# Performance work log

Measured on AMD Instinct MI355X. Metric: run time of the kernel, lower is better.

Reference implementation:

```python
import jax, jax.numpy as jnp
import numpy as np

MIN_PS = 4
MAX_PS = 16


def _enforce(mb):
    # mb: (L,) bool candidate boundaries (merge_signal < 0.7-quantile)
    # Faithful re-implementation of _enforce_patch_size_constraints:
    # walk boundaries left->right, skip segments < MIN_PS (start not advanced),
    # accept otherwise, and insert ceil(ps/MAX_PS)-1 evenly spaced splits for
    # oversized segments. seq_len-1 is always appended as a candidate.
    L = mb.shape[0]
    pos = jnp.arange(L, dtype=jnp.int32)
    cand = mb | (pos == L - 1)

    def fwd_step(start, inp):
        p, is_c = inp
        ps = p - start
        acc = is_c & (ps >= MIN_PS)
        k = jnp.where(acc, (ps + MAX_PS - 1) // MAX_PS, jnp.int32(1))
        sz = jnp.maximum(jnp.where(acc, ps // k, jnp.int32(1)), 1)
        new_start = jnp.where(acc, p, start)
        return new_start, (acc, start, sz, k)

    _, (acc, seg_start, sz, k) = jax.lax.scan(fwd_step, jnp.int32(0), (pos, cand))

    # Reverse scan: propagate each accepted boundary's (start, split_size, num_splits)
    # back to the interior positions of its segment so splits can be placed in parallel.
    def rev_step(carry, inp):
        a, s, z, kk = inp
        cs, cz, ck, cv = carry
        out = (cs, cz, ck, cv)
        ncarry = (jnp.where(a, s, cs), jnp.where(a, z, cz), jnp.where(a, kk, ck), cv | a)
        return ncarry, out

    init = (jnp.int32(0), jnp.int32(1), jnp.int32(1), jnp.bool_(False))
    _, (fs, fz, fk, fv) = jax.lax.scan(rev_step, init, (acc, seg_start, sz, k), reverse=True)
    r = pos - fs
    j = r // fz
    split = fv & (r > 0) & (r % fz == 0) & (j >= 1) & (j <= fk - 1)
    return acc | split


def reference(x, attention_mask, W1, b1, W2, b2, Wc, bc, Wb1, bb1, Wb2, bb2):
    B, L, D = x.shape
    # content scorer: Linear -> ReLU -> Linear -> Sigmoid
    content = jax.nn.sigmoid(jax.nn.relu(x @ W1 + b1) @ W2 + b2)[..., 0]  # (B, L)
    # grouped Conv1d(d, d//2, k=3, pad=1, groups=d//4)
    xc = jnp.transpose(x, (0, 2, 1))  # (B, D, L)
    pf = jax.lax.conv_general_dilated(xc, Wc, (1,), ((1, 1),),
                                      feature_group_count=D // 4,
                                      dimension_numbers=('NCH', 'OIH', 'NCH'))
    pf = jnp.transpose(pf + bc[None, :, None], (0, 2, 1))  # (B, L, D//2)
    comb = jnp.concatenate([x, pf], axis=-1)
    bscore = jax.nn.sigmoid(jax.nn.relu(comb @ Wb1 + bb1) @ Wb2 + bb2)[..., 0]  # (B, L)
    signal = content * (1.0 - bscore) * attention_mask
    thr = jnp.quantile(signal, 0.7, axis=1, keepdims=True)
    mb = signal < thr
    new_b = jax.vmap(_enforce)(mb)  # (B, L) bool, new_b[:,0] is always False

    # segment id per token = inclusive cumsum of boundaries
    seg = jnp.cumsum(new_b.astype(jnp.int32), axis=1)
    seg_flat = (seg + jnp.arange(B, dtype=jnp.int32)[:, None] * L).reshape(-1)
    NS = B * L
    xm = x * attention_mask[..., None]
    e = jnp.sum(xm * xm, axis=-1).reshape(-1)  # softmax logits = ||token||^2
    m = jax.ops.segment_max(e, seg_flat, num_segments=NS)
    w = jnp.exp(e - m[seg_flat])
    denom = jax.ops.segment_sum(w, seg_flat, num_segments=NS)
    wn = w / denom[seg_flat]
    merged = jax.ops.segment_sum(xm.reshape(-1, D) * wn[:, None], seg_flat,
                                 num_segments=NS).reshape(B, L, D)
    # segment_boundaries: 1 for every segment except the first, zero padding
    n_last = seg[:, -1]
    p = jnp.arange(L)
    seg_bounds = ((p[None, :] >= 1) & (p[None, :] <= n_last[:, None])).astype(jnp.float32)
    return merged, seg_bounds


def setup_inputs() -> dict:
    key = jax.random.key(0)
    B, L, D = 4, 8192, 512
    ks = jax.random.split(key, 8)
    s = 0.02
    return {
        'x': jax.random.normal(ks[0], (B, L, D), jnp.float32),
        'attention_mask': jnp.ones((B, L), jnp.float32),
        'W1': jax.random.normal(ks[1], (D, D // 4), jnp.float32) * s,
        'b1': jnp.zeros((D // 4,), jnp.float32),
        'W2': jax.random.normal(ks[2], (D // 4, 1), jnp.float32) * s,
        'b2': jnp.zeros((1,), jnp.float32),
        'Wc': jax.random.normal(ks[3], (D // 2, 4, 3), jnp.float32) * s,
        'bc': jnp.zeros((D // 2,), jnp.float32),
        'Wb1': jax.random.normal(ks[4], (D + D // 2, D // 4), jnp.float32) * s,
        'bb1': jnp.zeros((D // 4,), jnp.float32),
        'Wb2': jax.random.normal(ks[5], (D // 4, 1), jnp.float32) * s,
        'bb2': jnp.zeros((1,), jnp.float32),
    }
```

## Files before the change

kernel.cpp:

```cpp
#include <hip/hip_runtime.h>
#include <math.h>

#define B_  4
#define L_  8192
#define D_  512
#define BL_ (B_*L_)
#define TOK 64
#define XS  68
#define KC  16
#define NCH (D_/KC)

__global__ __launch_bounds__(256, 2) void k_signal(
    const float* __restrict__ x, const float* __restrict__ mask,
    const float* __restrict__ W1, const float* __restrict__ b1,
    const float* __restrict__ W2, const float* __restrict__ b2,
    const float* __restrict__ Wc, const float* __restrict__ bc,
    const float* __restrict__ Wb1, const float* __restrict__ bb1,
    const float* __restrict__ Wb2, const float* __restrict__ bb2,
    float* __restrict__ signal, float* __restrict__ e)
{
  __shared__ float ws1[KC][128];
  __shared__ float wsb[KC][128];
  __shared__ float wsp[8][128];
  __shared__ float xt[KC][XS];
  __shared__ float pf[8][XS];

  const int t   = threadIdx.x;
  const int blk = blockIdx.x;
  const int b   = blk >> 7;
  const int l0  = (blk & 127) << 6;
  const float* xb = x + (size_t)b * L_ * D_;

  const int jq = t & 31, tw = t >> 5;
  const int j0 = jq << 2, tok0 = tw << 3;

  const int stok = t >> 2, skk = t & 3;
  const int oo_c = t >> 5;
  const int m2   = (t & 31) << 1;
  const int cb_c = (oo_c >> 1) << 2;

  const int srow = t >> 5, sc4 = (t & 31) << 2;

  float a1[8][4], a2[8][4];
#pragma unroll
  for (int i = 0; i < 8; ++i)
#pragma unroll
    for (int j = 0; j < 4; ++j) { a1[i][j] = 0.f; a2[i][j] = 0.f; }
  float esacc = 0.f;

  float4 r_w1a, r_w1b, r_wba, r_wbb, r_wp, r_xv, r_hv;
  float4 r_wc0, r_wc1, r_wc2;
  float  r_bc;

  auto LOAD = [&](int c) {
    const int kc = c << 4;
    r_w1a = *reinterpret_cast<const float4*>(W1  + (size_t)(kc + srow) * 128 + sc4);
    r_w1b = *reinterpret_cast<const float4*>(W1  + (size_t)(kc + 8 + srow) * 128 + sc4);
    r_wba = *reinterpret_cast<const float4*>(Wb1 + (size_t)(kc + srow) * 128 + sc4);
    r_wbb = *reinterpret_cast<const float4*>(Wb1 + (size_t)(kc + 8 + srow) * 128 + sc4);
    r_wp  = *reinterpret_cast<const float4*>(Wb1 + (size_t)(512 + (c << 3) + srow) * 128 + sc4);
    r_xv  = *reinterpret_cast<const float4*>(xb + (size_t)(l0 + stok) * D_ + kc + (skk << 2));
    if (t < 8) {
      const int hh = t >> 2, kk = t & 3;
      const int l = hh ? (l0 + TOK) : (l0 - 1);
      r_hv = make_float4(0.f, 0.f, 0.f, 0.f);
      if (l >= 0 && l < L_)
        r_hv = *reinterpret_cast<const float4*>(xb + (size_t)l * D_ + kc + (kk << 2));
    }
    const int o = (c << 3) + oo_c;
    const float* wcp = Wc + o * 12;
    r_wc0 = *reinterpret_cast<const float4*>(wcp);
    r_wc1 = *reinterpret_cast<const float4*>(wcp + 4);
    r_wc2 = *reinterpret_cast<const float4*>(wcp + 8);
    r_bc  = bc[o];
  };

  LOAD(0);

  for (int c = 0; c < NCH; ++c) {
    __syncthreads();

    *reinterpret_cast<float4*>(&ws1[srow][sc4])     = r_w1a;
    *reinterpret_cast<float4*>(&ws1[8 + srow][sc4]) = r_w1b;
    *reinterpret_cast<float4*>(&wsb[srow][sc4])     = r_wba;
    *reinterpret_cast<float4*>(&wsb[8 + srow][sc4]) = r_wbb;
    *reinterpret_cast<float4*>(&wsp[srow][sc4])     = r_wp;
    {
      const float4 v = r_xv;
      esacc = fmaf(v.x, v.x, esacc); esacc = fmaf(v.y, v.y, esacc);
      esacc = fmaf(v.z, v.z, esacc); esacc = fmaf(v.w, v.w, esacc);
      const int r = skk << 2;
      xt[r + 0][stok] = v.x; xt[r + 1][stok] = v.y;
      xt[r + 2][stok] = v.z; xt[r + 3][stok] = v.w;
    }
    if (t < 8) {
      const int hh = t >> 2, kk = t & 3;
      const int col = TOK + hh, r = kk << 2;
      xt[r + 0][col] = r_hv.x; xt[r + 1][col] = r_hv.y;
      xt[r + 2][col] = r_hv.z; xt[r + 3][col] = r_hv.w;
    }
    __syncthreads();

    float wcl[12];
    wcl[0] = r_wc0.x; wcl[1]  = r_wc0.y; wcl[2]  = r_wc0.z; wcl[3]  = r_wc0.w;
    wcl[4] = r_wc1.x; wcl[5]  = r_wc1.y; wcl[6]  = r_wc1.z; wcl[7]  = r_wc1.w;
    wcl[8] = r_wc2.x; wcl[9]  = r_wc2.y; wcl[10] = r_wc2.z; wcl[11] = r_wc2.w;
    const float bcv = r_bc;

    if (c + 1 < NCH) LOAD(c + 1);

    {
      float pa = bcv, pb = bcv;
      const int tm1 = (m2 == 0) ? TOK : m2 - 1;
      const int tp2 = (m2 + 2 == TOK) ? TOK + 1 : m2 + 2;
#pragma unroll
      for (int i = 0; i < 4; ++i) {
        const float* row = &xt[cb_c + i][0];
        const float  xm1 = row[tm1];
        const float2 x01 = *reinterpret_cast<const float2*>(&row[m2]);
        const float  xp2 = row[tp2];
        pa = fmaf(xm1,   wcl[i * 3 + 0], pa);
        pa = fmaf(x01.x, wcl[i * 3 + 1], pa);
        pa = fmaf(x01.y, wcl[i * 3 + 2], pa);
        pb = fmaf(x01.x, wcl[i * 3 + 0], pb);
        pb = fmaf(x01.y, wcl[i * 3 + 1], pb);
        pb = fmaf(xp2,   wcl[i * 3 + 2], pb);
      }
      *reinterpret_cast<float2*>(&pf[oo_c][m2]) = make_float2(pa, pb);
    }

#pragma unroll 4
    for (int k = 0; k < KC; ++k) {
      const float4 w1 = *reinterpret_cast<const float4*>(&ws1[k][j0]);
      const float4 wb = *reinterpret_cast<const float4*>(&wsb[k][j0]);
      const float4 xa = *reinterpret_cast<const float4*>(&xt[k][tok0]);
      const float4 xc = *reinterpret_cast<const float4*>(&xt[k][tok0 + 4]);
      const float xs8[8] = {xa.x, xa.y, xa.z, xa.w, xc.x, xc.y, xc.z, xc.w};
#pragma unroll
      for (int i = 0; i < 8; ++i) {
        a1[i][0] = fmaf(xs8[i], w1.x, a1[i][0]);
        a1[i][1] = fmaf(xs8[i], w1.y, a1[i][1]);
        a1[i][2] = fmaf(xs8[i], w1.z, a1[i][2]);
        a1[i][3] = fmaf(xs8[i], w1.w, a1[i][3]);
        a2[i][0] = fmaf(xs8[i], wb.x, a2[i][0]);
        a2[i][1] = fmaf(xs8[i], wb.y, a2[i][1]);
        a2[i][2] = fmaf(xs8[i], wb.z, a2[i][2]);
        a2[i][3] = fmaf(xs8[i], wb.w, a2[i][3]);
      }
    }
    __syncthreads();

#pragma unroll 2
    for (int oo = 0; oo < 8; ++oo) {
      const float4 wp = *reinterpret_cast<const float4*>(&wsp[oo][j0]);
      const float4 pa4 = *reinterpret_cast<const float4*>(&pf[oo][tok0]);
      const float4 pb4 = *reinterpret_cast<const float4*>(&pf[oo][tok0 + 4]);
      const float ps8[8] = {pa4.x, pa4.y, pa4.z, pa4.w, pb4.x, pb4.y, pb4.z, pb4.w};
#pragma unroll
      for (int i = 0; i < 8; ++i) {
        a2[i][0] = fmaf(ps8[i], wp.x, a2[i][0]);
        a2[i][1] = fmaf(ps8[i], wp.y, a2[i][1]);
        a2[i][2] = fmaf(ps8[i], wp.z, a2[i][2]);
        a2[i][3] = fmaf(ps8[i], wp.w, a2[i][3]);
      }
    }
  }

  {
    float b1v[4], w2v[4], bbv[4], wv2[4];
#pragma unroll
    for (int jj = 0; jj < 4; ++jj) {
      b1v[jj] = b1[j0 + jj];  w2v[jj] = W2[j0 + jj];
      bbv[jj] = bb1[j0 + jj]; wv2[jj] = Wb2[j0 + jj];
    }
    const float bias2 = b2[0], biasb2 = bb2[0];
#pragma unroll
    for (int i = 0; i < 8; ++i) {
      float p1 = 0.f, p2 = 0.f;
#pragma unroll
      for (int jj = 0; jj < 4; ++jj) {
        const float h1 = a1[i][jj] + b1v[jj];
        if (h1 > 0.f) p1 = fmaf(h1, w2v[jj], p1);
        const float h2 = a2[i][jj] + bbv[jj];
        if (h2 > 0.f) p2 = fmaf(h2, wv2[jj], p2);
      }
#pragma unroll
      for (int off = 1; off < 32; off <<= 1) {
        p1 += __shfl_xor(p1, off, 64);
        p2 += __shfl_xor(p2, off, 64);
      }
      if (jq == 0) {
        const int gi = b * L_ + l0 + tok0 + i;
        const float content = 1.f / (1.f + expf(-(p1 + bias2)));
        const float bscore  = 1.f / (1.f + expf(-(p2 + biasb2)));
        signal[gi] = content * (1.f - bscore) * mask[gi];
      }
    }
  }

  {
    float es = esacc;
    es += __shfl_xor(es, 1, 64);
    es += __shfl_xor(es, 2, 64);
    if (skk == 0) {
      const int gi = b * L_ + l0 + stok;
      const float m = mask[gi];
      e[gi] = m * m * es;
    }
  }
}

__device__ __forceinline__ int chain_sim(unsigned long long w, int from) {
  int last = -1;
  while (from < 64) {
    const unsigned long long m = w & (~0ull << from);
    if (m == 0ull) break;
    const int p = __ffsll(m) - 1;
    last = p;
    from = p + 4;
  }
  return last;
}

__global__ __launch_bounds__(1024) void k_select(
    const float* __restrict__ signal,
    int* __restrict__ starts, int* __restrict__ nlast)
{
  __shared__ unsigned int bins[4][256];
  __shared__ unsigned int sel_prefix;
  __shared__ int sel_rank;
  __shared__ float sh_thr;
  __shared__ unsigned int wmin[16];
  __shared__ int wcnt[16];
  __shared__ unsigned long long cw[128];
  __shared__ unsigned char nb[L_];
  __shared__ signed char tbl[128][4];
  __shared__ int st_in[128];
  __shared__ int offs[257];

  const int b = blockIdx.x, t = threadIdx.x;
  const int wv = t >> 6, lane = t & 63;
  const float* s = signal + b * L_;

  float val[8];
  unsigned int key[8];
#pragma unroll
  for (int i = 0; i < 8; ++i) {
    val[i] = s[(i << 10) + t];
    const unsigned int u = __float_as_uint(val[i]);
    key[i] = (u & 0x80000000u) ? ~u : (u | 0x80000000u);
  }

  if (t == 0) { sel_prefix = 0u; sel_rank = 5733; }
  __syncthreads();
  for (int round = 0; round < 4; ++round) {
    reinterpret_cast<unsigned int*>(bins)[t] = 0u;
    __syncthreads();
    const unsigned int pre = sel_prefix;
    const int shift = 24 - 8 * round;
#pragma unroll
    for (int i = 0; i < 8; ++i) {
      if (round == 0 || (key[i] >> (shift + 8)) == pre)
        atomicAdd(&bins[t >> 8][(key[i] >> shift) & 255u], 1u);
    }
    __syncthreads();
    if (t < 256)
      bins[0][t] = bins[0][t] + bins[1][t] + bins[2][t] + bins[3][t];
    __syncthreads();
    if (t < 64) {
      const unsigned int c0 = bins[0][(t << 2) + 0], c1 = bins[0][(t << 2) + 1];
      const unsigned int c2 = bins[0][(t << 2) + 2], c3 = bins[0][(t << 2) + 3];
      const unsigned int lsum = c0 + c1 + c2 + c3;
      unsigned int run = lsum;
#pragma unroll
      for (int off = 1; off < 64; off <<= 1) {
        const unsigned int v = __shfl_up(run, off, 64);
        if (t >= off) run += v;
      }
      const int r = sel_rank;
      if (r >= (int)(run - lsum) && r < (int)run) {
        int rr = r - (int)(run - lsum);
        unsigned int cbin;
        if (rr < (int)c0) { cbin = 0; }
        else if (rr < (int)(c0 + c1)) { cbin = 1; rr -= (int)c0; }
        else if (rr < (int)(c0 + c1 + c2)) { cbin = 2; rr -= (int)(c0 + c1); }
        else { cbin = 3; rr -= (int)(c0 + c1 + c2); }
        sel_rank = rr;
        sel_prefix = (pre << 8) | ((unsigned int)(t << 2) | cbin);
      }
    }
    __syncthreads();
  }
  const unsigned int k0 = sel_prefix;

  {
    int cle = 0;
    unsigned int mgt = 0xFFFFFFFFu;
#pragma unroll
    for (int i = 0; i < 8; ++i) {
      if (key[i] <= k0) ++cle;
      else mgt = min(mgt, key[i]);
    }
#pragma unroll
    for (int off = 1; off < 64; off <<= 1) {
      cle += __shfl_xor(cle, off, 64);
      mgt = min(mgt, (unsigned int)__shfl_xor((int)mgt, off, 64));
    }
    if (lane == 0) { wcnt[wv] = cle; wmin[wv] = mgt; }
    __syncthreads();
    if (t == 0) {
      int C = 0; unsigned int M = 0xFFFFFFFFu;
      for (int g = 0; g < 16; ++g) { C += wcnt[g]; M = min(M, wmin[g]); }
      const unsigned int k1 = (C >= 5735) ? k0 : M;
      const unsigned int u0 = (k0 & 0x80000000u) ? (k0 & 0x7fffffffu) : ~k0;
      const unsigned int u1 = (k1 & 0x80000000u) ? (k1 & 0x7fffffffu) : ~k1;
      const float v0 = __uint_as_float(u0);
      const float v1 = __uint_as_float(u1);
      const float g = 0.7f * 8191.0f - 5733.0f;
      sh_thr = v0 + g * (v1 - v0);
    }
    __syncthreads();
  }
  const float thr = sh_thr;

#pragma unroll
  for (int i = 0; i < 8; ++i) {
    const unsigned long long m = __ballot(val[i] < thr);
    if (lane == 0) cw[(i << 4) + wv] = m;
  }
  {
    const int base = t << 3;
#pragma unroll
    for (int i = 0; i < 8; ++i) nb[base + i] = 0;
  }
  __syncthreads();
  if (t == 0) cw[127] |= (1ull << 63);
  __syncthreads();

  if (t < 512) {
    const int blk = t >> 2, cls = t & 3;
    tbl[blk][cls] = (signed char)chain_sim(cw[blk], cls);
  }
  __syncthreads();

  if (t == 0) {
    int st = 0;
    for (int blk = 0; blk < 128; ++blk) {
      const int bs = blk << 6;
      st_in[blk] = st;
      int pl;
      if (blk == 0) {
        pl = chain_sim(cw[0], 4);
      } else {
        int off = st + 4 - bs;
        if (off < 0) off = 0;
        pl = tbl[blk][off];
      }
      if (pl >= 0) st = bs + pl;
    }
  }
  __syncthreads();

  if (t < 128) {
    const int bs = t << 6;
    const unsigned long long w = cw[t];
    int st = st_in[t];
    int from = st + 4 - bs;
    if (from < 0) from = 0;
    while (from < 64) {
      const unsigned long long m = w & (~0ull << from);
      if (m == 0ull) break;
      const int p_rel = __ffsll(m) - 1;
      const int p = bs + p_rel;
      nb[p] = 1;
      const int ps = p - st;
      const int k = (ps + 15) >> 4;
      if (k > 1) {
        int sz = ps / k; if (sz < 1) sz = 1;
        for (int j = 1; j < k; ++j) nb[st + j * sz] = 1;
      }
      st = p;
      from = p_rel + 4;
    }
  }
  __syncthreads();

  int ls = 0, run = 0;
  if (t < 256) {
    const int base = t << 5;
    for (int i = 0; i < 32; ++i) ls += nb[base + i];
    run = ls;
#pragma unroll
    for (int off = 1; off < 64; off <<= 1) {
      const int v = __shfl_up(run, off, 64);
      if ((t & 63) >= off) run += v;
    }
    if ((t & 63) == 63) wcnt[t >> 6] = run;
  }
  __syncthreads();
  if (t < 256) {
    const int w = t >> 6;
    int addb = 0;
    if (w > 0) addb += wcnt[0];
    if (w > 1) addb += wcnt[1];
    if (w > 2) addb += wcnt[2];
    offs[t] = addb + run - ls;
    if (t == 255) offs[256] = addb + run;
  }
  __syncthreads();
  if (t < 256) {
    const int base = t << 5;
    int rn = offs[t];
    for (int i = 0; i < 32; ++i) {
      rn += nb[base + i];
      if (nb[base + i]) starts[b * L_ + rn] = base + i;
    }
  }
  if (t == 0) { starts[b * L_ + 0] = 0; nlast[b] = offs[256]; }
}

__global__ __launch_bounds__(256) void k_merge(const float* __restrict__ x,
    const float* __restrict__ mask, const float* __restrict__ e,
    const int* __restrict__ starts, const int* __restrict__ nlast,
    float* __restrict__ merged, float* __restrict__ bounds)
{
  const int idx = (blockIdx.x << 2) + (threadIdx.x >> 6);
  const int b   = idx >> 13;
  const int sid = idx & (L_ - 1);
  const int n = nlast[b];
  const int lane = threadIdx.x & 63;
  if (lane == 0)
    bounds[(size_t)b * L_ + sid] = (sid >= 1 && sid <= n) ? 1.0f : 0.0f;
  const int c0 = lane << 3;
  float* o = merged + (size_t)(b * L_ + sid) * D_ + c0;
  if (sid > n) {
    const float4 z = make_float4(0.f, 0.f, 0.f, 0.f);
    reinterpret_cast<float4*>(o)[0] = z;
    reinterpret_cast<float4*>(o)[1] = z;
    return;
  }
  const int t0 = starts[b * L_ + sid];
  const int t1 = (sid < n) ? starts[b * L_ + sid + 1] : L_;
  const int len = t1 - t0;
  const float* eb = e + b * L_;

  float acc[8] = {0,0,0,0,0,0,0,0};

  if (len <= 64) {
    const float ev = (lane < len) ? eb[t0 + lane] : -INFINITY;
    float mx = ev;
#pragma unroll
    for (int off = 1; off < 64; off <<= 1)
      mx = fmaxf(mx, __shfl_xor(mx, off, 64));
    const float ex = expf(ev - mx);
    float den = ex;
#pragma unroll
    for (int off = 1; off < 64; off <<= 1)
      den += __shfl_xor(den, off, 64);
    const float mk = (lane < len) ? mask[b * L_ + t0 + lane] : 0.f;
    const float scl = (ex / den) * mk;

    const float* xr = x + (size_t)(b * L_ + t0) * D_ + c0;
    float4 u0 = reinterpret_cast<const float4*>(xr)[0];
    float4 u1 = reinterpret_cast<const float4*>(xr)[1];
    for (int r = 0; r < len; ++r) {
      float4 n0, n1;
      if (r + 1 < len) {
        const float* xn = xr + (size_t)(r + 1) * D_;
        n0 = reinterpret_cast<const float4*>(xn)[0];
        n1 = reinterpret_cast<const float4*>(xn)[1];
      }
      const float sc = __shfl(scl, r, 64);
      acc[0] = fmaf(sc, u0.x, acc[0]); acc[1] = fmaf(sc, u0.y, acc[1]);
      acc[2] = fmaf(sc, u0.z, acc[2]); acc[3] = fmaf(sc, u0.w, acc[3]);
      acc[4] = fmaf(sc, u1.x, acc[4]); acc[5] = fmaf(sc, u1.y, acc[5]);
      acc[6] = fmaf(sc, u1.z, acc[6]); acc[7] = fmaf(sc, u1.w, acc[7]);
      u0 = n0; u1 = n1;
    }
  } else {
    float mx = -INFINITY;
    for (int p = t0; p < t1; ++p) mx = fmaxf(mx, eb[p]);
    float den = 0.f;
    for (int p = t0; p < t1; ++p) den += expf(eb[p] - mx);
    for (int p = t0; p < t1; ++p) {
      const float wn = expf(eb[p] - mx) / den;
      const float sc = wn * mask[b * L_ + p];
      const float* xr = x + ((size_t)(b * L_ + p)) * D_ + c0;
      const float4 u0 = reinterpret_cast<const float4*>(xr)[0];
      const float4 u1 = reinterpret_cast<const float4*>(xr)[1];
      acc[0] = fmaf(sc, u0.x, acc[0]); acc[1] = fmaf(sc, u0.y, acc[1]);
      acc[2] = fmaf(sc, u0.z, acc[2]); acc[3] = fmaf(sc, u0.w, acc[3]);
      acc[4] = fmaf(sc, u1.x, acc[4]); acc[5] = fmaf(sc, u1.y, acc[5]);
      acc[6] = fmaf(sc, u1.z, acc[6]); acc[7] = fmaf(sc, u1.w, acc[7]);
    }
  }
  reinterpret_cast<float4*>(o)[0] = make_float4(acc[0], acc[1], acc[2], acc[3]);
  reinterpret_cast<float4*>(o)[1] = make_float4(acc[4], acc[5], acc[6], acc[7]);
}

extern "C" void kernel_launch(void* const* d_in, const int* in_sizes, int n_in,
                              void* d_out, int out_size, void* d_ws, size_t ws_size,
                              hipStream_t stream) {
  (void)in_sizes; (void)n_in; (void)out_size; (void)ws_size;
  const float* x    = (const float*)d_in[0];
  const float* mask = (const float*)d_in[1];
  const float* W1   = (const float*)d_in[2];
  const float* b1   = (const float*)d_in[3];
  const float* W2   = (const float*)d_in[4];
  const float* b2   = (const float*)d_in[5];
  const float* Wc   = (const float*)d_in[6];
  const float* bc   = (const float*)d_in[7];
  const float* Wb1  = (const float*)d_in[8];
  const float* bb1  = (const float*)d_in[9];
  const float* Wb2  = (const float*)d_in[10];
  const float* bb2  = (const float*)d_in[11];

  float* merged = (float*)d_out;
  float* bounds = (float*)d_out + (size_t)BL_ * D_;

  char* ws = (char*)d_ws;
  float* signal = (float*)(ws);
  float* e      = (float*)(ws + (size_t)BL_ * 4);
  int*   starts = (int*)  (ws + (size_t)BL_ * 8);
  int*   nlast  = (int*)  (ws + (size_t)BL_ * 12);

  k_signal<<<BL_ / TOK, 256, 0, stream>>>(x, mask, W1, b1, W2, b2, Wc, bc,
                                          Wb1, bb1, Wb2, bb2, signal, e);
  k_select<<<B_, 1024, 0, stream>>>(signal, starts, nlast);
  k_merge<<<BL_ / 4, 256, 0, stream>>>(x, mask, e, starts, nlast, merged, bounds);
}
```

Baseline: 301.5 us.

## Build top-byte histogram in signal kernel and pre-zero merged output there

The signal kernel now builds a per-batch histogram of the top radix byte of the signal keys in shared memory and adds it into a global histogram. This lets the select kernel skip its first radix-select round. The signal kernel also zero-fills its slice of the merged and bounds outputs while it computes, so the merge kernel can return early for padded segments instead of writing zeros. This moves the 64 MB zero-fill into a compute-bound kernel, where it may overlap with compute. The cost is a memset launch, extra global atomics, and extra store traffic during the signal kernel.

Measured after the change: 299.8 us. Within noise of the previous version (-0.6%).

```diff
diff --git a/kernel.cpp b/kernel.cpp
--- a/kernel.cpp
+++ b/kernel.cpp
@@ -17,7 +17,9 @@
     const float* __restrict__ Wc, const float* __restrict__ bc,
     const float* __restrict__ Wb1, const float* __restrict__ bb1,
     const float* __restrict__ Wb2, const float* __restrict__ bb2,
-    float* __restrict__ signal, float* __restrict__ e)
+    float* __restrict__ signal, float* __restrict__ e,
+    unsigned int* __restrict__ hist,
+    float* __restrict__ merged, float* __restrict__ bounds)
 {
   __shared__ float ws1[KC][128];
   __shared__ float wsb[KC][128];
@@ -40,6 +42,12 @@
   const int cb_c = (oo_c >> 1) << 2;
 
   const int srow = t >> 5, sc4 = (t & 31) << 2;
+
+  if (t < 16) {
+    float4* bz = reinterpret_cast<float4*>(bounds + (size_t)b * L_ + l0);
+    bz[t] = make_float4(0.f, 0.f, 0.f, 0.f);
+  }
+  float4* mz = reinterpret_cast<float4*>(merged + (size_t)(b * L_ + l0) * D_);
 
   float a1[8][4], a2[8][4];
 #pragma unroll
@@ -109,6 +117,8 @@
 
     if (c + 1 < NCH) LOAD(c + 1);
 
+    mz[(c << 8) + t] = make_float4(0.f, 0.f, 0.f, 0.f);
+
     {
       float pa = bcv, pb = bcv;
       const int tm1 = (m2 == 0) ? TOK : m2 - 1;
@@ -166,6 +176,9 @@
     }
   }
 
+  float sigv[8];
+#pragma unroll
+  for (int i = 0; i < 8; ++i) sigv[i] = 0.f;
   {
     float b1v[4], w2v[4], bbv[4], wv2[4];
 #pragma unroll
@@ -193,7 +206,9 @@
         const int gi = b * L_ + l0 + tok0 + i;
         const float content = 1.f / (1.f + expf(-(p1 + bias2)));
         const float bscore  = 1.f / (1.f + expf(-(p2 + biasb2)));
-        signal[gi] = content * (1.f - bscore) * mask[gi];
+        const float s = content * (1.f - bscore) * mask[gi];
+        sigv[i] = s;
+        signal[gi] = s;
       }
     }
   }
@@ -208,6 +223,24 @@
       e[gi] = m * m * es;
     }
   }
+
+  {
+    __syncthreads();
+    unsigned int* hl = reinterpret_cast<unsigned int*>(&xt[0][0]);
+    hl[t & 255] = 0u;
+    __syncthreads();
+    if (jq == 0) {
+#pragma unroll
+      for (int i = 0; i < 8; ++i) {
+        const unsigned int u = __float_as_uint(sigv[i]);
+        const unsigned int key = (u & 0x80000000u) ? ~u : (u | 0x80000000u);
+        atomicAdd(&hl[key >> 24], 1u);
+      }
+    }
+    __syncthreads();
+    const unsigned int cnt = hl[t & 255];
+    if (cnt) atomicAdd(&hist[(b << 8) + (t & 255)], cnt);
+  }
 }
 
 __device__ __forceinline__ int chain_sim(unsigned long long w, int from) {
@@ -223,7 +256,7 @@
 }
 
 __global__ __launch_bounds__(1024) void k_select(
-    const float* __restrict__ signal,
+    const float* __restrict__ signal, const unsigned int* __restrict__ hist,
     int* __restrict__ starts, int* __restrict__ nlast)
 {
   __shared__ unsigned int bins[4][256];
@@ -251,16 +284,40 @@
     key[i] = (u & 0x80000000u) ? ~u : (u | 0x80000000u);
   }
 
-  if (t == 0) { sel_prefix = 0u; sel_rank = 5733; }
-  __syncthreads();
-  for (int round = 0; round < 4; ++round) {
+  if (t < 256) bins[0][t] = hist[(b << 8) + t];
+  __syncthreads();
+  if (t < 64) {
+    const unsigned int c0 = bins[0][(t << 2) + 0], c1 = bins[0][(t << 2) + 1];
+    const unsigned int c2 = bins[0][(t << 2) + 2], c3 = bins[0][(t << 2) + 3];
+    const unsigned int lsum = c0 + c1 + c2 + c3;
+    unsigned int run = lsum;
+#pragma unroll
+    for (int off = 1; off < 64; off <<= 1) {
+      const unsigned int v = __shfl_up(run, off, 64);
+      if (t >= off) run += v;
+    }
+    const int r = 5733;
+    if (r >= (int)(run - lsum) && r < (int)run) {
+      int rr = r - (int)(run - lsum);
+      unsigned int cbin;
+      if (rr < (int)c0) { cbin = 0; }
+      else if (rr < (int)(c0 + c1)) { cbin = 1; rr -= (int)c0; }
+      else if (rr < (int)(c0 + c1 + c2)) { cbin = 2; rr -= (int)(c0 + c1); }
+      else { cbin = 3; rr -= (int)(c0 + c1 + c2); }
+      sel_rank = rr;
+      sel_prefix = (unsigned int)(t << 2) | cbin;
+    }
+  }
+  __syncthreads();
+
+  for (int round = 1; round < 4; ++round) {
     reinterpret_cast<unsigned int*>(bins)[t] = 0u;
     __syncthreads();
     const unsigned int pre = sel_prefix;
     const int shift = 24 - 8 * round;
 #pragma unroll
     for (int i = 0; i < 8; ++i) {
-      if (round == 0 || (key[i] >> (shift + 8)) == pre)
+      if ((key[i] >> (shift + 8)) == pre)
         atomicAdd(&bins[t >> 8][(key[i] >> shift) & 255u], 1u);
     }
     __syncthreads();
@@ -428,17 +485,12 @@
   const int b   = idx >> 13;
   const int sid = idx & (L_ - 1);
   const int n = nlast[b];
+  if (sid > n) return;
   const int lane = threadIdx.x & 63;
-  if (lane == 0)
-    bounds[(size_t)b * L_ + sid] = (sid >= 1 && sid <= n) ? 1.0f : 0.0f;
+  if (lane == 0 && sid >= 1)
+    bounds[(size_t)b * L_ + sid] = 1.0f;
   const int c0 = lane << 3;
   float* o = merged + (size_t)(b * L_ + sid) * D_ + c0;
-  if (sid > n) {
-    const float4 z = make_float4(0.f, 0.f, 0.f, 0.f);
-    reinterpret_cast<float4*>(o)[0] = z;
-    reinterpret_cast<float4*>(o)[1] = z;
-    return;
-  }
   const int t0 = starts[b * L_ + sid];
   const int t1 = (sid < n) ? starts[b * L_ + sid + 1] : L_;
   const int len = t1 - t0;
@@ -519,13 +571,16 @@
   float* bounds = (float*)d_out + (size_t)BL_ * D_;
 
   char* ws = (char*)d_ws;
-  float* signal = (float*)(ws);
-  float* e      = (float*)(ws + (size_t)BL_ * 4);
-  int*   starts = (int*)  (ws + (size_t)BL_ * 8);
-  int*   nlast  = (int*)  (ws + (size_t)BL_ * 12);
-
+  float*        signal = (float*)(ws);
+  float*        e      = (float*)(ws + (size_t)BL_ * 4);
+  int*          starts = (int*)  (ws + (size_t)BL_ * 8);
+  int*          nlast  = (int*)  (ws + (size_t)BL_ * 12);
+  unsigned int* hist   = (unsigned int*)(ws + (size_t)BL_ * 12 + 256);
+
+  hipMemsetAsync(hist, 0, B_ * 256 * sizeof(unsigned int), stream);
   k_signal<<<BL_ / TOK, 256, 0, stream>>>(x, mask, W1, b1, W2, b2, Wc, bc,
-                                          Wb1, bb1, Wb2, bb2, signal, e);
-  k_select<<<B_, 1024, 0, stream>>>(signal, starts, nlast);
+                                          Wb1, bb1, Wb2, bb2, signal, e,
+                                          hist, merged, bounds);
+  k_select<<<B_, 1024, 0, stream>>>(signal, hist, starts, nlast);
   k_merge<<<BL_ / 4, 256, 0, stream>>>(x, mask, e, starts, nlast, merged, bounds);
 }
```
